# Kernel tuning notes

Measured on AMD Instinct MI355X. Metric: run time of the kernel, lower is better.

## Reference

```python
import jax, jax.numpy as jnp
import numpy as np

B, S, D, H = 4, 2048, 1024, 16
DK = D // H


def setup_inputs() -> dict:
    key = jax.random.key(0)
    ks = jax.random.split(key, 12)
    s = 1.0 / np.sqrt(D)
    inp = {
        "query": jax.random.normal(ks[0], (B, S, D), jnp.float32),
        "key": jax.random.normal(ks[1], (B, S, D), jnp.float32),
        "value": jax.random.normal(ks[2], (B, S, D), jnp.float32),
        "mask": jax.random.randint(ks[3], (B, S, S), 0, 2, jnp.int32),
        "Wq": jax.random.uniform(ks[4], (D, D), jnp.float32, -s, s),
        "bq": jax.random.uniform(ks[5], (D,), jnp.float32, -s, s),
        "Wk": jax.random.uniform(ks[6], (D, D), jnp.float32, -s, s),
        "bk": jax.random.uniform(ks[7], (D,), jnp.float32, -s, s),
        "Wv": jax.random.uniform(ks[8], (D, D), jnp.float32, -s, s),
        "bv": jax.random.uniform(ks[9], (D,), jnp.float32, -s, s),
        "Wo": jax.random.uniform(ks[10], (D, D), jnp.float32, -s, s),
        "bo": jax.random.uniform(ks[11], (D,), jnp.float32, -s, s),
    }
    return inp


def reference(query, key, value, mask, Wq, bq, Wk, bk, Wv, bv, Wo, bo):
    # Linear projections (torch Linear: x @ W.T + b), split into heads: [B,H,S,DK]
    def proj(x, W, b):
        y = x @ W.T + b
        return y.reshape(B, S, H, DK).transpose(0, 2, 1, 3)

    q = proj(query, Wq, bq)
    k = proj(key, Wk, bk)
    v = proj(value, Wv, bv)

    # scores: [B,H,S,S]
    scores = jnp.einsum("bhqd,bhkd->bhqk", q, k) / jnp.sqrt(jnp.float32(DK))
    m = mask[:, None, :, :]  # broadcast over heads
    scores = jnp.where(m == 0, jnp.float32(-1e9), scores)
    attn = jax.nn.softmax(scores, axis=-1)
    out = jnp.einsum("bhqk,bhkd->bhqd", attn, v)
    out = out.transpose(0, 2, 1, 3).reshape(B, S, D)
    return out @ Wo.T + bo
```

## Files before the change

kernel.cpp:

```cpp
#include <hip/hip_runtime.h>

#define B_  4
#define S_  2048
#define D_  1024
#define H_  16
#define DK_ 64

typedef __attribute__((ext_vector_type(8))) __bf16 bf16x8;
typedef __attribute__((ext_vector_type(4))) float  f32x4;

#define AS1 __attribute__((address_space(1)))
#define AS3 __attribute__((address_space(3)))

__device__ __forceinline__ void gl2lds16(const void* g, void* l) {
    __builtin_amdgcn_global_load_lds((const AS1 unsigned int*)g,
                                     (AS3 unsigned int*)l, 16, 0, 0);
}

__device__ __forceinline__ unsigned short f2bf(float f) {
    union { float f; unsigned u; } v; v.f = f;
    return (unsigned short)((v.u + 0x7FFFu + ((v.u >> 16) & 1u)) >> 16);
}

__device__ __forceinline__ unsigned cvt_pk_bf16(float lo, float hi) {
    unsigned r;
    asm("v_cvt_pk_bf16_f32 %0, %1, %2" : "=v"(r) : "v"(lo), "v"(hi));
    return r;
}

__device__ __forceinline__ void cast8(const float* __restrict__ x,
                                      unsigned short* __restrict__ y, int i) {
    float4 a = ((const float4*)x)[2 * i];
    float4 b = ((const float4*)x)[2 * i + 1];
    uint4 w;
    w.x = cvt_pk_bf16(a.x, a.y);
    w.y = cvt_pk_bf16(a.z, a.w);
    w.z = cvt_pk_bf16(b.x, b.y);
    w.w = cvt_pk_bf16(b.z, b.w);
    ((uint4*)y)[i] = w;
}

__global__ __launch_bounds__(256) void cast_act(
    const float* __restrict__ a, const float* __restrict__ b,
    const float* __restrict__ c, unsigned short* __restrict__ ya,
    unsigned short* __restrict__ yb, unsigned short* __restrict__ yc)
{
    const int sel = blockIdx.y;
    const float* x = (sel == 0) ? a : (sel == 1) ? b : c;
    unsigned short* y = (sel == 0) ? ya : (sel == 1) ? yb : yc;
    cast8(x, y, blockIdx.x * 256 + threadIdx.x);
}

__global__ __launch_bounds__(256) void cast_w(
    const float* __restrict__ a, const float* __restrict__ b,
    const float* __restrict__ c, const float* __restrict__ d,
    unsigned short* __restrict__ ya, unsigned short* __restrict__ yb,
    unsigned short* __restrict__ yc, unsigned short* __restrict__ yd)
{
    const int sel = blockIdx.y;
    const float* x = (sel == 0) ? a : (sel == 1) ? b : (sel == 2) ? c : d;
    unsigned short* y = (sel == 0) ? ya : (sel == 1) ? yb : (sel == 2) ? yc : yd;
    cast8(x, y, blockIdx.x * 256 + threadIdx.x);
}

__global__ __launch_bounds__(256, 3) void gemm_qkv(
    const unsigned short* __restrict__ Xq, const unsigned short* __restrict__ Xk,
    const unsigned short* __restrict__ Xv, const unsigned short* __restrict__ Wqkv,
    const float* __restrict__ bq, const float* __restrict__ bk,
    const float* __restrict__ bv, unsigned short* __restrict__ Qw,
    unsigned short* __restrict__ Kw, unsigned short* __restrict__ Vt,
    float qscale)
{
    __shared__ unsigned short As[128 * 64];
    __shared__ unsigned short Bs[128 * 64];

    const int tid  = threadIdx.x;
    const int lane = tid & 63, wave = tid >> 6;
    const int l16  = lane & 15, quad = lane >> 4;
    const int wm = wave & 1, wn = wave >> 1;

    const int lin  = blockIdx.y * 24 + blockIdx.x;
    const int slin = (lin & 7) * 192 + (lin >> 3);
    const int bx = slin % 24, by = slin / 24;

    const int n0 = bx * 128, m0 = by * 128;
    const int xr = l16 & 7;

    const int sel = bx >> 3;
    const unsigned short* X = (sel == 0) ? Xq : (sel == 1) ? Xk : Xv;

    const int row8 = lane >> 3;
    const int sc   = ((lane & 7) ^ row8) * 8;

    f32x4 acc[4][4] = {};

    for (int k0 = 0; k0 < D_; k0 += 64) {
        __syncthreads();
        #pragma unroll
        for (int j = 0; j < 4; ++j) {
            const int ca = wave * 4 + j;
            const int r  = ca * 8 + row8;
            gl2lds16(X    + (size_t)(m0 + r) * D_ + k0 + sc, &As[ca * 512 + (lane & 63) * 8]);
            gl2lds16(Wqkv + (size_t)(n0 + r) * D_ + k0 + sc, &Bs[ca * 512 + (lane & 63) * 8]);
        }
        __syncthreads();

        #pragma unroll
        for (int s = 0; s < 2; ++s) {
            bf16x8 a[4], bb[4];
            #pragma unroll
            for (int i = 0; i < 4; ++i)
                a[i] = *(const bf16x8*)&As[(wm * 64 + i * 16 + l16) * 64 + (((s * 4 + quad) ^ xr)) * 8];
            #pragma unroll
            for (int j = 0; j < 4; ++j)
                bb[j] = *(const bf16x8*)&Bs[(wn * 64 + j * 16 + l16) * 64 + (((s * 4 + quad) ^ xr)) * 8];
            #pragma unroll
            for (int i = 0; i < 4; ++i)
                #pragma unroll
                for (int j = 0; j < 4; ++j)
                    acc[i][j] = __builtin_amdgcn_mfma_f32_16x16x32_bf16(a[i], bb[j], acc[i][j], 0, 0, 0);
        }
    }

    const int ncol = (bx & 7) * 128 + wn * 64;
    const float scale = (sel == 0) ? qscale : 1.0f;
    const float* bias = (sel == 0) ? bq : (sel == 1) ? bk : bv;

    if (sel == 2) {
        const int bb_ = m0 >> 11;
        #pragma unroll
        for (int j = 0; j < 4; ++j) {
            const int dk = ncol + j * 16 + l16;
            const float bvv = bias[dk];
            #pragma unroll
            for (int i = 0; i < 4; ++i) {
                const int sb = (m0 & (S_ - 1)) + wm * 64 + i * 16 + quad * 4;
                uint2 w;
                w.x = cvt_pk_bf16(acc[i][j][0] + bvv, acc[i][j][1] + bvv);
                w.y = cvt_pk_bf16(acc[i][j][2] + bvv, acc[i][j][3] + bvv);
                *(uint2*)(Vt + (size_t)(bb_ * D_ + dk) * S_ + sb) = w;
            }
        }
    } else {
        unsigned short* Outp = sel ? Kw : Qw;
        #pragma unroll
        for (int j = 0; j < 4; ++j) {
            const int n = ncol + j * 16 + l16;
            const float bvv = bias[n];
            #pragma unroll
            for (int i = 0; i < 4; ++i) {
                #pragma unroll
                for (int r = 0; r < 4; ++r) {
                    const int m = m0 + wm * 64 + i * 16 + quad * 4 + r;
                    Outp[(size_t)m * D_ + n] = f2bf((acc[i][j][r] + bvv) * scale);
                }
            }
        }
    }
}

__global__ __launch_bounds__(256, 3) void gemm_out(
    const unsigned short* __restrict__ X, const unsigned short* __restrict__ W,
    const float* __restrict__ bias, float* __restrict__ Out)
{
    __shared__ unsigned short As[128 * 64];
    __shared__ unsigned short Bs[128 * 64];

    const int tid  = threadIdx.x;
    const int lane = tid & 63, wave = tid >> 6;
    const int l16  = lane & 15, quad = lane >> 4;
    const int wm = wave & 1, wn = wave >> 1;

    const int lin  = blockIdx.y * 8 + blockIdx.x;
    const int slin = (lin & 7) * 64 + (lin >> 3);
    const int bx = slin & 7, by = slin >> 3;

    const int n0 = bx * 128, m0 = by * 128;
    const int xr = l16 & 7;

    const int row8 = lane >> 3;
    const int sc   = ((lane & 7) ^ row8) * 8;

    f32x4 acc[4][4] = {};

    for (int k0 = 0; k0 < D_; k0 += 64) {
        __syncthreads();
        #pragma unroll
        for (int j = 0; j < 4; ++j) {
            const int ca = wave * 4 + j;
            const int r  = ca * 8 + row8;
            gl2lds16(X + (size_t)(m0 + r) * D_ + k0 + sc, &As[ca * 512 + (lane & 63) * 8]);
            gl2lds16(W + (size_t)(n0 + r) * D_ + k0 + sc, &Bs[ca * 512 + (lane & 63) * 8]);
        }
        __syncthreads();

        #pragma unroll
        for (int s = 0; s < 2; ++s) {
            bf16x8 a[4], bb[4];
            #pragma unroll
            for (int i = 0; i < 4; ++i)
                a[i] = *(const bf16x8*)&As[(wm * 64 + i * 16 + l16) * 64 + (((s * 4 + quad) ^ xr)) * 8];
            #pragma unroll
            for (int j = 0; j < 4; ++j)
                bb[j] = *(const bf16x8*)&Bs[(wn * 64 + j * 16 + l16) * 64 + (((s * 4 + quad) ^ xr)) * 8];
            #pragma unroll
            for (int i = 0; i < 4; ++i)
                #pragma unroll
                for (int j = 0; j < 4; ++j)
                    acc[i][j] = __builtin_amdgcn_mfma_f32_16x16x32_bf16(a[i], bb[j], acc[i][j], 0, 0, 0);
        }
    }

    #pragma unroll
    for (int j = 0; j < 4; ++j) {
        const int n = n0 + wn * 64 + j * 16 + l16;
        const float bv = bias[n];
        #pragma unroll
        for (int i = 0; i < 4; ++i) {
            #pragma unroll
            for (int r = 0; r < 4; ++r) {
                const int m = m0 + wm * 64 + i * 16 + quad * 4 + r;
                Out[(size_t)m * D_ + n] = acc[i][j][r] + bv;
            }
        }
    }
}

__global__ __launch_bounds__(256) void pack_mask(
    const int* __restrict__ mask, unsigned long long* __restrict__ pm)
{
    const int gid  = blockIdx.x * 256 + threadIdx.x;
    const int w    = gid >> 6;
    const int lane = threadIdx.x & 63;
    const int mv = mask[(size_t)w * 64 + lane];
    const unsigned long long bal = __ballot(mv != 0);
    if (lane == 0) pm[w] = bal;
}

__global__ __launch_bounds__(256, 4) void attn_kernel(
    const unsigned short* __restrict__ Q,
    const unsigned short* __restrict__ Kg,
    const unsigned short* __restrict__ Vt,
    const unsigned long long* __restrict__ pm,
    unsigned short* __restrict__ O)
{
    __shared__ unsigned short Ks[64 * 64];
    __shared__ unsigned short Vs[2][64 * 64];
    __shared__ unsigned short Ps[128 * 64];

    const int tid  = threadIdx.x;
    const int lane = tid & 63, wave = tid >> 6;
    const int l16  = lane & 15, quad = lane >> 4;

    const int n  = blockIdx.y * 16 + blockIdx.x;
    const int ns = (n & 7) * 128 + (n >> 3);
    const int b  = ns >> 8;
    const int h  = (ns >> 4) & 15;
    const int q0 = (ns & 15) * 128;
    const int xq = l16 & 7;

    union { uint4 u; bf16x8 v; } ones_u;
    ones_u.u = make_uint4(0x3F803F80u, 0x3F803F80u, 0x3F803F80u, 0x3F803F80u);
    const bf16x8 vb_ones = ones_u.v;

    bf16x8 qa[2][2];
    #pragma unroll
    for (int qf = 0; qf < 2; ++qf) {
        const unsigned short* qp =
            Q + (size_t)(b * S_ + q0 + wave * 32 + qf * 16 + l16) * D_ + h * DK_ + quad * 8;
        qa[qf][0] = *(const bf16x8*)qp;
        qa[qf][1] = *(const bf16x8*)(qp + 32);
    }

    const unsigned short* Kbase = Kg + (size_t)(b * S_) * D_ + h * DK_;
    const unsigned short* Vbase = Vt + (size_t)(b * D_ + h * DK_) * S_;

    auto stageK = [&](int kt2) {
        const int k0 = kt2 * 64;
        #pragma unroll
        for (int j = 0; j < 2; ++j) {
            const int c = j * 256 + tid;
            const int row = c >> 3;
            const int cl = (c & 7) ^ (row & 7);
            gl2lds16(Kbase + (size_t)(k0 + row) * D_ + cl * 8, &Ks[c * 8]);
        }
    };
    auto stageV = [&](int bi2, int kt2) {
        const int k0 = kt2 * 64;
        #pragma unroll
        for (int j = 0; j < 2; ++j) {
            const int c = j * 256 + tid;
            const int row = c >> 3;
            const int cl = (c & 7) ^ (row & 7);
            gl2lds16(Vbase + (size_t)row * S_ + k0 + cl * 8, &Vs[bi2][c * 8]);
        }
    };

    const unsigned long long* pmq0 =
        pm + (size_t)(b * S_ + q0 + wave * 32 + l16) * (S_ / 64);
    const unsigned long long* pmq1 = pmq0 + (size_t)16 * (S_ / 64);

    f32x4 oacc[2][5] = {};

    stageK(0);
    stageV(0, 0);
    __syncthreads();

    int bi = 0;
    for (int kt = 0; kt < S_ / 64; ++kt) {
        const bool more = (kt + 1 < S_ / 64);
        const unsigned long long wq0 = pmq0[kt];
        const unsigned long long wq1 = pmq1[kt];
        if (more) stageV(bi ^ 1, kt + 1);

        #pragma unroll
        for (int half = 0; half < 2; ++half) {
            f32x4 sct[2][2] = {};
            __builtin_amdgcn_s_setprio(1);
            #pragma unroll
            for (int s = 0; s < 2; ++s) {
                const int cs = ((s * 4 + quad) ^ xq) * 8;
                #pragma unroll
                for (int mbh = 0; mbh < 2; ++mbh) {
                    bf16x8 ka = *(const bf16x8*)&Ks[((half * 2 + mbh) * 16 + l16) * 64 + cs];
                    sct[mbh][0] = __builtin_amdgcn_mfma_f32_16x16x32_bf16(ka, qa[0][s], sct[mbh][0], 0, 0, 0);
                    sct[mbh][1] = __builtin_amdgcn_mfma_f32_16x16x32_bf16(ka, qa[1][s], sct[mbh][1], 0, 0, 0);
                }
            }
            __builtin_amdgcn_s_setprio(0);

            #pragma unroll
            for (int qf = 0; qf < 2; ++qf) {
                const unsigned long long wq = qf ? wq1 : wq0;
                #pragma unroll
                for (int mbh = 0; mbh < 2; ++mbh) {
                    const int mb = half * 2 + mbh;
                    const unsigned nib = (unsigned)(wq >> (mb * 16 + quad * 4)) & 0xFu;
                    float e[4];
                    #pragma unroll
                    for (int r = 0; r < 4; ++r) {
                        float x = __builtin_amdgcn_exp2f(sct[mbh][qf][r]);
                        e[r] = ((nib >> r) & 1u) ? x : 0.f;
                    }
                    uint2 w;
                    w.x = cvt_pk_bf16(e[0], e[1]);
                    w.y = cvt_pk_bf16(e[2], e[3]);
                    *(uint2*)&Ps[(wave * 32 + qf * 16 + l16) * 64 +
                                 ((mb * 16 + quad * 4) ^ (xq * 8))] = w;
                }
            }
        }

        __syncthreads();
        if (more) stageK(kt + 1);

        __builtin_amdgcn_s_setprio(1);
        #pragma unroll
        for (int s = 0; s < 2; ++s) {
            const int cs = ((s * 4 + quad) ^ xq) * 8;
            bf16x8 pa0 = *(const bf16x8*)&Ps[(wave * 32 + l16) * 64 +
                                             ((s * 32 + quad * 8) ^ (xq * 8))];
            bf16x8 pa1 = *(const bf16x8*)&Ps[(wave * 32 + 16 + l16) * 64 +
                                             ((s * 32 + quad * 8) ^ (xq * 8))];
            #pragma unroll
            for (int db = 0; db < 4; ++db) {
                bf16x8 vb = *(const bf16x8*)&Vs[bi][(db * 16 + l16) * 64 + cs];
                oacc[0][db] = __builtin_amdgcn_mfma_f32_16x16x32_bf16(pa0, vb, oacc[0][db], 0, 0, 0);
                oacc[1][db] = __builtin_amdgcn_mfma_f32_16x16x32_bf16(pa1, vb, oacc[1][db], 0, 0, 0);
            }
            oacc[0][4] = __builtin_amdgcn_mfma_f32_16x16x32_bf16(pa0, vb_ones, oacc[0][4], 0, 0, 0);
            oacc[1][4] = __builtin_amdgcn_mfma_f32_16x16x32_bf16(pa1, vb_ones, oacc[1][4], 0, 0, 0);
        }
        __builtin_amdgcn_s_setprio(0);

        __syncthreads();
        bi ^= 1;
    }

    #pragma unroll
    for (int qf = 0; qf < 2; ++qf) {
        #pragma unroll
        for (int r = 0; r < 4; ++r) {
            const float linv = 1.0f / oacc[qf][4][r];
            const int qg = q0 + wave * 32 + qf * 16 + quad * 4 + r;
            #pragma unroll
            for (int db = 0; db < 4; ++db) {
                O[(size_t)(b * S_ + qg) * D_ + h * DK_ + db * 16 + l16] =
                    f2bf(oacc[qf][db][r] * linv);
            }
        }
    }
}

extern "C" void kernel_launch(void* const* d_in, const int* in_sizes, int n_in,
                              void* d_out, int out_size, void* d_ws, size_t ws_size,
                              hipStream_t stream)
{
    const float* q   = (const float*)d_in[0];
    const float* k   = (const float*)d_in[1];
    const float* v   = (const float*)d_in[2];
    const int* mask  = (const int*)d_in[3];
    const float* Wq  = (const float*)d_in[4];
    const float* bq  = (const float*)d_in[5];
    const float* Wk  = (const float*)d_in[6];
    const float* bk  = (const float*)d_in[7];
    const float* Wv  = (const float*)d_in[8];
    const float* bv  = (const float*)d_in[9];
    const float* Wo  = (const float*)d_in[10];
    const float* bo  = (const float*)d_in[11];

    const size_t MN = (size_t)B_ * S_ * D_;
    const size_t WN = (size_t)D_ * D_;
    unsigned short* qb  = (unsigned short*)d_ws;
    unsigned short* kb  = qb + MN;
    unsigned short* vb  = kb + MN;
    unsigned short* Qw  = vb + MN;
    unsigned short* Kw  = Qw + MN;
    unsigned short* Vt  = Kw + MN;
    unsigned short* wqb = Vt + MN;
    unsigned short* wkb = wqb + WN;
    unsigned short* wvb = wkb + WN;
    unsigned short* wob = wvb + WN;
    unsigned short* Ow  = qb;
    unsigned long long* pm = (unsigned long long*)d_out;

    dim3 blk(256);
    const int actBlocks = (int)(MN / 8 / 256);
    const int wBlocks   = (int)(WN / 8 / 256);

    pack_mask<<<(B_ * S_ * S_) / 256, blk, 0, stream>>>(mask, pm);

    cast_act<<<dim3(actBlocks, 3), blk, 0, stream>>>(q, k, v, qb, kb, vb);
    cast_w<<<dim3(wBlocks, 4), blk, 0, stream>>>(Wq, Wk, Wv, Wo, wqb, wkb, wvb, wob);

    const float qscale = 1.44269504088896341f * 0.125f;

    gemm_qkv<<<dim3(3 * D_ / 128, (B_ * S_) / 128), blk, 0, stream>>>(
        qb, kb, vb, wqb, bq, bk, bv, Qw, Kw, Vt, qscale);

    attn_kernel<<<dim3(S_ / 128, B_ * H_), blk, 0, stream>>>(Qw, Kw, Vt, pm, Ow);

    gemm_out<<<dim3(D_ / 128, (B_ * S_) / 128), blk, 0, stream>>>(
        Ow, wob, bo, (float*)d_out);
}
```

Before: 398.3 us.

## Fuse casts and mask packing into one prep kernel; remap GEMM tile order

Replaces the three preprocessing launches (mask packing, activation cast, weight cast) with a single prep_all kernel. The mask-packing blocks now each loop over 32 chunks instead of one chunk per block. Both GEMM kernels also get a new block-to-tile mapping that groups 4 column tiles by 8 row tiles per XCD, aiming for better L2 reuse of A and W tiles. This saves launch overhead and lets the memory-bound prep work overlap, at the cost of uneven per-block work within the fused kernel.

New measurement: 395.7 us. About the same (-0.6%).

```diff
diff --git a/kernel.cpp b/kernel.cpp
--- a/kernel.cpp
+++ b/kernel.cpp
@@ -40,27 +40,39 @@
     ((uint4*)y)[i] = w;
 }
 
-__global__ __launch_bounds__(256) void cast_act(
-    const float* __restrict__ a, const float* __restrict__ b,
-    const float* __restrict__ c, unsigned short* __restrict__ ya,
-    unsigned short* __restrict__ yb, unsigned short* __restrict__ yc)
+__global__ __launch_bounds__(256) void prep_all(
+    const float* __restrict__ q, const float* __restrict__ k,
+    const float* __restrict__ v, const float* __restrict__ Wq,
+    const float* __restrict__ Wk, const float* __restrict__ Wv,
+    const float* __restrict__ Wo, const int* __restrict__ mask,
+    unsigned short* __restrict__ qb, unsigned short* __restrict__ kb,
+    unsigned short* __restrict__ vb, unsigned short* __restrict__ wqb,
+    unsigned short* __restrict__ wkb, unsigned short* __restrict__ wvb,
+    unsigned short* __restrict__ wob, unsigned long long* __restrict__ pmo)
 {
-    const int sel = blockIdx.y;
-    const float* x = (sel == 0) ? a : (sel == 1) ? b : c;
-    unsigned short* y = (sel == 0) ? ya : (sel == 1) ? yb : yc;
-    cast8(x, y, blockIdx.x * 256 + threadIdx.x);
-}
-
-__global__ __launch_bounds__(256) void cast_w(
-    const float* __restrict__ a, const float* __restrict__ b,
-    const float* __restrict__ c, const float* __restrict__ d,
-    unsigned short* __restrict__ ya, unsigned short* __restrict__ yb,
-    unsigned short* __restrict__ yc, unsigned short* __restrict__ yd)
-{
-    const int sel = blockIdx.y;
-    const float* x = (sel == 0) ? a : (sel == 1) ? b : (sel == 2) ? c : d;
-    unsigned short* y = (sel == 0) ? ya : (sel == 1) ? yb : (sel == 2) ? yc : yd;
-    cast8(x, y, blockIdx.x * 256 + threadIdx.x);
+    const int bid = blockIdx.x;
+    if (bid < 12288) {
+        const int sel = bid >> 12;
+        const float* x = (sel == 0) ? q : (sel == 1) ? k : v;
+        unsigned short* y = (sel == 0) ? qb : (sel == 1) ? kb : vb;
+        cast8(x, y, (bid & 4095) * 256 + threadIdx.x);
+    } else if (bid < 14336) {
+        const int b2 = bid - 12288;
+        const int sel = b2 >> 9;
+        const float* x = (sel == 0) ? Wq : (sel == 1) ? Wk : (sel == 2) ? Wv : Wo;
+        unsigned short* y = (sel == 0) ? wqb : (sel == 1) ? wkb : (sel == 2) ? wvb : wob;
+        cast8(x, y, (b2 & 511) * 256 + threadIdx.x);
+    } else {
+        const int b3 = bid - 14336;
+        const int lane = threadIdx.x & 63;
+        int w = (b3 * 256 + (int)threadIdx.x) >> 6;
+        #pragma unroll 4
+        for (int it = 0; it < 32; ++it, w += 8192) {
+            const int mv = mask[(size_t)w * 64 + lane];
+            const unsigned long long bal = __ballot(mv != 0);
+            if (lane == 0) pmo[w] = bal;
+        }
+    }
 }
 
 __global__ __launch_bounds__(256, 3) void gemm_qkv(
@@ -79,9 +91,13 @@
     const int l16  = lane & 15, quad = lane >> 4;
     const int wm = wave & 1, wn = wave >> 1;
 
-    const int lin  = blockIdx.y * 24 + blockIdx.x;
-    const int slin = (lin & 7) * 192 + (lin >> 3);
-    const int bx = slin % 24, by = slin / 24;
+    const int lin = blockIdx.y * 24 + blockIdx.x;
+    const int xcd = lin & 7;
+    const int i   = lin >> 3;
+    const int ng  = i >> 5;
+    const int r_  = i & 31;
+    const int bx  = ng * 4 + (r_ & 3);
+    const int by  = xcd * 8 + (r_ >> 2);
 
     const int n0 = bx * 128, m0 = by * 128;
     const int xr = l16 & 7;
@@ -109,16 +125,16 @@
         for (int s = 0; s < 2; ++s) {
             bf16x8 a[4], bb[4];
             #pragma unroll
-            for (int i = 0; i < 4; ++i)
-                a[i] = *(const bf16x8*)&As[(wm * 64 + i * 16 + l16) * 64 + (((s * 4 + quad) ^ xr)) * 8];
+            for (int i2 = 0; i2 < 4; ++i2)
+                a[i2] = *(const bf16x8*)&As[(wm * 64 + i2 * 16 + l16) * 64 + (((s * 4 + quad) ^ xr)) * 8];
             #pragma unroll
             for (int j = 0; j < 4; ++j)
                 bb[j] = *(const bf16x8*)&Bs[(wn * 64 + j * 16 + l16) * 64 + (((s * 4 + quad) ^ xr)) * 8];
             #pragma unroll
-            for (int i = 0; i < 4; ++i)
+            for (int i2 = 0; i2 < 4; ++i2)
                 #pragma unroll
                 for (int j = 0; j < 4; ++j)
-                    acc[i][j] = __builtin_amdgcn_mfma_f32_16x16x32_bf16(a[i], bb[j], acc[i][j], 0, 0, 0);
+                    acc[i2][j] = __builtin_amdgcn_mfma_f32_16x16x32_bf16(a[i2], bb[j], acc[i2][j], 0, 0, 0);
         }
     }
 
@@ -133,11 +149,11 @@
             const int dk = ncol + j * 16 + l16;
             const float bvv = bias[dk];
             #pragma unroll
-            for (int i = 0; i < 4; ++i) {
-                const int sb = (m0 & (S_ - 1)) + wm * 64 + i * 16 + quad * 4;
+            for (int i2 = 0; i2 < 4; ++i2) {
+                const int sb = (m0 & (S_ - 1)) + wm * 64 + i2 * 16 + quad * 4;
                 uint2 w;
-                w.x = cvt_pk_bf16(acc[i][j][0] + bvv, acc[i][j][1] + bvv);
-                w.y = cvt_pk_bf16(acc[i][j][2] + bvv, acc[i][j][3] + bvv);
+                w.x = cvt_pk_bf16(acc[i2][j][0] + bvv, acc[i2][j][1] + bvv);
+                w.y = cvt_pk_bf16(acc[i2][j][2] + bvv, acc[i2][j][3] + bvv);
                 *(uint2*)(Vt + (size_t)(bb_ * D_ + dk) * S_ + sb) = w;
             }
         }
@@ -148,11 +164,11 @@
             const int n = ncol + j * 16 + l16;
             const float bvv = bias[n];
             #pragma unroll
-            for (int i = 0; i < 4; ++i) {
+            for (int i2 = 0; i2 < 4; ++i2) {
                 #pragma unroll
                 for (int r = 0; r < 4; ++r) {
-                    const int m = m0 + wm * 64 + i * 16 + quad * 4 + r;
-                    Outp[(size_t)m * D_ + n] = f2bf((acc[i][j][r] + bvv) * scale);
+                    const int m = m0 + wm * 64 + i2 * 16 + quad * 4 + r;
+                    Outp[(size_t)m * D_ + n] = f2bf((acc[i2][j][r] + bvv) * scale);
                 }
             }
         }
@@ -171,9 +187,13 @@
     const int l16  = lane & 15, quad = lane >> 4;
     const int wm = wave & 1, wn = wave >> 1;
 
-    const int lin  = blockIdx.y * 8 + blockIdx.x;
-    const int slin = (lin & 7) * 64 + (lin >> 3);
-    const int bx = slin & 7, by = slin >> 3;
+    const int lin = blockIdx.y * 8 + blockIdx.x;
+    const int xcd = lin & 7;
+    const int i   = lin >> 3;
+    const int ng  = i >> 5;
+    const int r_  = i & 31;
+    const int bx  = ng * 4 + (r_ & 3);
+    const int by  = xcd * 8 + (r_ >> 2);
 
     const int n0 = bx * 128, m0 = by * 128;
     const int xr = l16 & 7;
@@ -198,16 +218,16 @@
         for (int s = 0; s < 2; ++s) {
             bf16x8 a[4], bb[4];
             #pragma unroll
-            for (int i = 0; i < 4; ++i)
-                a[i] = *(const bf16x8*)&As[(wm * 64 + i * 16 + l16) * 64 + (((s * 4 + quad) ^ xr)) * 8];
+            for (int i2 = 0; i2 < 4; ++i2)
+                a[i2] = *(const bf16x8*)&As[(wm * 64 + i2 * 16 + l16) * 64 + (((s * 4 + quad) ^ xr)) * 8];
             #pragma unroll
             for (int j = 0; j < 4; ++j)
                 bb[j] = *(const bf16x8*)&Bs[(wn * 64 + j * 16 + l16) * 64 + (((s * 4 + quad) ^ xr)) * 8];
             #pragma unroll
-            for (int i = 0; i < 4; ++i)
+            for (int i2 = 0; i2 < 4; ++i2)
                 #pragma unroll
                 for (int j = 0; j < 4; ++j)
-                    acc[i][j] = __builtin_amdgcn_mfma_f32_16x16x32_bf16(a[i], bb[j], acc[i][j], 0, 0, 0);
+                    acc[i2][j] = __builtin_amdgcn_mfma_f32_16x16x32_bf16(a[i2], bb[j], acc[i2][j], 0, 0, 0);
         }
     }
 
@@ -216,25 +236,14 @@
         const int n = n0 + wn * 64 + j * 16 + l16;
         const float bv = bias[n];
         #pragma unroll
-        for (int i = 0; i < 4; ++i) {
+        for (int i2 = 0; i2 < 4; ++i2) {
             #pragma unroll
             for (int r = 0; r < 4; ++r) {
-                const int m = m0 + wm * 64 + i * 16 + quad * 4 + r;
-                Out[(size_t)m * D_ + n] = acc[i][j][r] + bv;
-            }
-        }
-    }
-}
-
-__global__ __launch_bounds__(256) void pack_mask(
-    const int* __restrict__ mask, unsigned long long* __restrict__ pm)
-{
-    const int gid  = blockIdx.x * 256 + threadIdx.x;
-    const int w    = gid >> 6;
-    const int lane = threadIdx.x & 63;
-    const int mv = mask[(size_t)w * 64 + lane];
-    const unsigned long long bal = __ballot(mv != 0);
-    if (lane == 0) pm[w] = bal;
+                const int m = m0 + wm * 64 + i2 * 16 + quad * 4 + r;
+                Out[(size_t)m * D_ + n] = acc[i2][j][r] + bv;
+            }
+        }
+    }
 }
 
 __global__ __launch_bounds__(256, 4) void attn_kernel(
@@ -425,13 +434,10 @@
     unsigned long long* pm = (unsigned long long*)d_out;
 
     dim3 blk(256);
-    const int actBlocks = (int)(MN / 8 / 256);
-    const int wBlocks   = (int)(WN / 8 / 256);
-
-    pack_mask<<<(B_ * S_ * S_) / 256, blk, 0, stream>>>(mask, pm);
-
-    cast_act<<<dim3(actBlocks, 3), blk, 0, stream>>>(q, k, v, qb, kb, vb);
-    cast_w<<<dim3(wBlocks, 4), blk, 0, stream>>>(Wq, Wk, Wv, Wo, wqb, wkb, wvb, wob);
+
+    prep_all<<<dim3(16384), blk, 0, stream>>>(
+        q, k, v, Wq, Wk, Wv, Wo, mask,
+        qb, kb, vb, wqb, wkb, wvb, wob, pm);
 
     const float qscale = 1.44269504088896341f * 0.125f;
 
```
